# Performance work log

Measured on AMD Instinct MI355X. Metric: run time of the kernel, lower is better.

The kernel has to match this reference:

```python
import jax, jax.numpy as jnp
import numpy as np

N_STATE = 2048
N_HEAD = 16
HEAD_DIM = N_STATE // N_HEAD  # 128
ROPE_THETA = 10000.0


def setup_inputs() -> dict:
    key = jax.random.key(0)
    ks = jax.random.split(key, 8)
    B, S, D = 2, 2048, N_STATE
    scale = 1.0 / np.sqrt(D)
    x = jax.random.normal(ks[0], (B, S, D), dtype=jnp.float32)
    Wq = jax.random.normal(ks[1], (D, D), dtype=jnp.float32) * scale
    bq = jnp.zeros((D,), dtype=jnp.float32)
    Wk = jax.random.normal(ks[2], (D, D), dtype=jnp.float32) * scale  # key has no bias
    Wv = jax.random.normal(ks[3], (D, D), dtype=jnp.float32) * scale
    bv = jnp.zeros((D,), dtype=jnp.float32)
    Wo = jax.random.normal(ks[4], (D, D), dtype=jnp.float32) * scale
    bo = jnp.zeros((D,), dtype=jnp.float32)
    return {"x": x, "Wq": Wq, "bq": bq, "Wk": Wk, "Wv": Wv, "bv": bv, "Wo": Wo, "bo": bo}


def _rope(t, pos):
    # t: [B, S, H, hd]; torchtune-style interleaved rotary (pairs of adjacent dims)
    hd = t.shape[-1]
    inv_freq = 1.0 / (ROPE_THETA ** (jnp.arange(0, hd, 2, dtype=jnp.float32) / hd))  # [hd/2]
    ang = pos[:, None] * inv_freq[None, :]                    # [S, hd/2]
    cos = jnp.cos(ang)[None, :, None, :].astype(t.dtype)       # [1,S,1,hd/2]
    sin = jnp.sin(ang)[None, :, None, :].astype(t.dtype)
    t1 = t[..., 0::2]
    t2 = t[..., 1::2]
    rot = jnp.stack([t1 * cos - t2 * sin, t2 * cos + t1 * sin], axis=-1)
    return rot.reshape(t.shape)


def reference(x, Wq, bq, Wk, Wv, bv, Wo, bo):
    B, S, D = x.shape
    H, hd = N_HEAD, D // N_HEAD
    q = (x @ Wq.T + bq).reshape(B, S, H, hd)
    k = (x @ Wk.T).reshape(B, S, H, hd)
    v = (x @ Wv.T + bv).reshape(B, S, H, hd)
    pos = jnp.arange(S, dtype=jnp.float32)
    q = _rope(q, pos)
    k = _rope(k, pos)
    # [B,H,S,hd]
    q = q.transpose(0, 2, 1, 3)
    k = k.transpose(0, 2, 1, 3)
    v = v.transpose(0, 2, 1, 3)
    scale = 1.0 / jnp.sqrt(jnp.asarray(hd, dtype=x.dtype))
    scores = jnp.einsum('bhqd,bhkd->bhqk', q, k) * scale       # [B,H,S,S]
    causal = jnp.tril(jnp.ones((S, S), dtype=bool))
    scores = jnp.where(causal[None, None], scores, jnp.finfo(scores.dtype).min)
    probs = jax.nn.softmax(scores, axis=-1)
    a = jnp.einsum('bhqk,bhkd->bhqd', probs, v)                # [B,H,S,hd]
    a = a.transpose(0, 2, 1, 3).reshape(B, S, D)
    return a @ Wo.T + bo
```

## Files before the change

kernel.cpp:

```cpp
#include <hip/hip_runtime.h>
#include <stdint.h>

typedef float f32x4 __attribute__((ext_vector_type(4)));
typedef __bf16 bf16x8 __attribute__((ext_vector_type(8)));
typedef unsigned short us8 __attribute__((ext_vector_type(8)));
typedef unsigned short us4 __attribute__((ext_vector_type(4)));
typedef unsigned int u32;

#define MFMA16(A, B, C) __builtin_amdgcn_mfma_f32_16x16x32_bf16( \
    __builtin_bit_cast(bf16x8, (A)), __builtin_bit_cast(bf16x8, (B)), (C), 0, 0, 0)

__device__ __forceinline__ unsigned short f2bf(float f) {
  u32 u = __builtin_bit_cast(u32, f);
  u = u + 0x7fffu + ((u >> 16) & 1u);
  return (unsigned short)(u >> 16);
}
__device__ __forceinline__ float bf2f(unsigned short b) {
  u32 u = ((u32)b) << 16;
  return __builtin_bit_cast(float, u);
}
__device__ __forceinline__ void gload16(const void* g, void* lds) {
  __builtin_amdgcn_global_load_lds((const __attribute__((address_space(1))) u32*)g,
                                   (__attribute__((address_space(3))) u32*)lds, 16, 0, 0);
}

__global__ __launch_bounds__(256) void convert_all(
    const float* __restrict__ x, const float* __restrict__ wq, const float* __restrict__ wk,
    const float* __restrict__ wv, const float* __restrict__ wo,
    unsigned short* __restrict__ xb, unsigned short* __restrict__ wcat,
    unsigned short* __restrict__ wob) {
  int tid = blockIdx.x * 256 + threadIdx.x;
  int nth = gridDim.x * 256;
  const float* srcs[5] = {x, wq, wk, wv, wo};
  unsigned short* dsts[5] = {xb, wcat, wcat + 4194304, wcat + 8388608, wob};
  const int n4s[5] = {2097152, 1048576, 1048576, 1048576, 1048576};
#pragma unroll
  for (int sg = 0; sg < 5; ++sg) {
    const float4* s = (const float4*)srcs[sg];
    us4* d = (us4*)dsts[sg];
    int n4 = n4s[sg];
    for (int i = tid; i < n4; i += nth) {
      float4 v = s[i];
      us4 o;
      o[0] = f2bf(v.x); o[1] = f2bf(v.y); o[2] = f2bf(v.z); o[3] = f2bf(v.w);
      d[i] = o;
    }
  }
}

template <int EPI>
__global__ __launch_bounds__(512, 2) void gemm8(
    const unsigned short* __restrict__ A, const unsigned short* __restrict__ B,
    int nTN, int N,
    float* __restrict__ outF, const float* __restrict__ bias,
    unsigned short* __restrict__ qb, unsigned short* __restrict__ kb,
    unsigned short* __restrict__ vtb, const float* __restrict__ bq,
    const float* __restrict__ bv) {
  constexpr int KT = 32;
  __shared__ alignas(16) char L[131072];
  char* Lp = L;
  int bid = (int)blockIdx.x, nwg = (int)gridDim.x;
  {
    int qq = nwg >> 3;
    int xcd = bid & 7, idx = bid >> 3;
    bid = xcd * qq + idx;
  }
  int tm = bid / nTN, tn = bid % nTN;
  int t = (int)threadIdx.x, l = t & 63, w = t >> 6;
  int g = l >> 4, ln = l & 15;
  int wr = w >> 2, wc = w & 3;
  const unsigned short* pA = A + (size_t)(tm * 256 + l) * 2048 + w * 8;
  const unsigned short* pB = B + (size_t)(tn * 256 + l) * 2048 + w * 8;

  f32x4 acc[2][2][4][2] = {};
  us8 af[4][2], bf[2][2][2];

#define FENCE asm volatile("" ::: "memory")
#define BAR do { FENCE; __builtin_amdgcn_s_barrier(); FENCE; } while (0)
#define VMW_(n) asm volatile("s_waitcnt vmcnt(" #n ")" ::: "memory")
#define VMW(n) VMW_(n)
#define HT(op, h, kt, bufsel) do { if ((kt) < KT) {                           \
    char* lb = Lp + (bufsel) * 65536 + (op) * 32768 + (h) * 16384 + w * 2048; \
    const unsigned short* gs = ((op) ? pB : pA) +                             \
        (size_t)((h) * 128) * 2048 + (size_t)(kt) * 64;                       \
    gload16(gs, lb);                                                          \
    gload16(gs + (size_t)64 * 2048, lb + 1024);                               \
  } } while (0)
#define RD_A(mh_, bufsel) do {                                                \
    _Pragma("unroll") for (int mf = 0; mf < 4; ++mf)                          \
    _Pragma("unroll") for (int kc = 0; kc < 2; ++kc)                          \
      af[mf][kc] = *(const us8*)(Lp + (bufsel) * 65536 + wr * 16384 +         \
          (kc * 4 + g) * 2048 + ((mh_) * 64 + mf * 16 + ln) * 16);            \
  } while (0)
#define RD_B(nh_, bufsel) do {                                                \
    _Pragma("unroll") for (int nf = 0; nf < 2; ++nf)                          \
    _Pragma("unroll") for (int kc = 0; kc < 2; ++kc)                          \
      bf[nh_][nf][kc] = *(const us8*)(Lp + (bufsel) * 65536 + 32768 +         \
          (wc >> 1) * 16384 + (kc * 4 + g) * 2048 +                           \
          ((wc & 1) * 64 + (nh_) * 32 + nf * 16 + ln) * 16);                  \
  } while (0)
#define MM(mh_, nh_) do {                                                     \
    __builtin_amdgcn_s_setprio(1);                                            \
    _Pragma("unroll") for (int mf = 0; mf < 4; ++mf)                          \
    _Pragma("unroll") for (int nf = 0; nf < 2; ++nf)                          \
    _Pragma("unroll") for (int kc = 0; kc < 2; ++kc)                          \
      acc[mh_][nh_][mf][nf] = MFMA16(af[mf][kc], bf[nh_][nf][kc],             \
                                     acc[mh_][nh_][mf][nf]);                  \
    __builtin_amdgcn_s_setprio(0);                                            \
  } while (0)
#define TILE(kt, b, VM) do {                                                  \
   RD_A(0, b); RD_B(0, b); RD_B(1, b);                                 \
          HT(0, 1, (kt) + 1, (b) ^ 1);                                        \
          BAR; MM(0, 0); BAR;                                                 \
   HT(1, 0, (kt) + 2, b);                                              \
          BAR; MM(0, 1); BAR;                                                 \
   RD_A(1, b);                                                         \
          HT(1, 1, (kt) + 2, b);                                              \
          BAR; MM(1, 0); BAR;                                                 \
   HT(0, 0, (kt) + 2, b);                                              \
          MM(1, 1); VMW(VM); BAR;                                             \
} while (0)

  HT(0, 0, 0, 0); HT(1, 0, 0, 0); HT(1, 1, 0, 0);
  HT(0, 1, 0, 0); HT(1, 0, 1, 1); HT(1, 1, 1, 1); HT(0, 0, 1, 1);
  VMW(6); BAR;

#pragma unroll 1
  for (int it = 0; it < 15; ++it) {
    TILE(2 * it, 0, 6);
    TILE(2 * it + 1, 1, 6);
  }
  TILE(30, 0, 0);
  TILE(31, 1, 0);

#undef TILE
#undef MM
#undef RD_B
#undef RD_A
#undef HT
#undef VMW
#undef VMW_
#undef BAR
#undef FENCE

  if (EPI == 1) {
#pragma unroll
    for (int mh = 0; mh < 2; ++mh)
#pragma unroll
    for (int nh = 0; nh < 2; ++nh)
#pragma unroll
    for (int mf = 0; mf < 4; ++mf)
#pragma unroll
    for (int nf = 0; nf < 2; ++nf) {
      int n = tn * 256 + wc * 64 + nh * 32 + nf * 16 + ln;
      float bz = bias[n];
      int m0 = tm * 256 + wr * 128 + mh * 64 + mf * 16 + g * 4;
#pragma unroll
      for (int r = 0; r < 4; ++r)
        outF[(size_t)(m0 + r) * N + n] = acc[mh][nh][mf][nf][r] + bz;
    }
  } else {
#pragma unroll
    for (int mh = 0; mh < 2; ++mh)
#pragma unroll
    for (int nh = 0; nh < 2; ++nh)
#pragma unroll
    for (int mf = 0; mf < 4; ++mf)
#pragma unroll
    for (int nf = 0; nf < 2; ++nf) {
      int n6 = tn * 256 + wc * 64 + nh * 32 + nf * 16 + ln;
      int sel = n6 >> 11, d = n6 & 2047, h = d >> 7, hd = d & 127;
      int m0 = tm * 256 + wr * 128 + mh * 64 + mf * 16 + g * 4;
      int b = m0 >> 11, s0 = m0 & 2047;
      if (sel == 2) {
        float badd = bv[d];
        us4 pk;
#pragma unroll
        for (int r = 0; r < 4; ++r) pk[r] = f2bf(acc[mh][nh][mf][nf][r] + badd);
        *(us4*)&vtb[((size_t)(b * 16 + h) * 128 + hd) * 2048 + s0] = pk;
      } else {
        unsigned short* dst = sel ? kb : qb;
        float badd = sel ? 0.f : bq[d];
#pragma unroll
        for (int r = 0; r < 4; ++r)
          dst[((size_t)(b * 16 + h) * 2048 + (s0 + r)) * 128 + hd] =
              f2bf(acc[mh][nh][mf][nf][r] + badd);
      }
    }
  }
}

template <int EPI>
__global__ __launch_bounds__(512, 2) void gemm2(
    const unsigned short* __restrict__ A, const unsigned short* __restrict__ B,
    int nTN, int N,
    float* __restrict__ outF, const float* __restrict__ bias) {
  constexpr int K = 2048, KT = 64;
  __shared__ alignas(16) char L[4 * 24576];
  int bid = (int)blockIdx.x, nwg = (int)gridDim.x;
  {
    int qq = nwg >> 3;
    int xcd = bid & 7, idx = bid >> 3;
    bid = xcd * qq + idx;
  }
  int tm = bid / nTN, tn = bid % nTN;
  int t = (int)threadIdx.x, l = t & 63, w = t >> 6;
  int g = l >> 4, ln = l & 15;
  int wr = w >> 2, wc = w & 3;
  const unsigned short* Ab =
      A + (size_t)(tm * 128 + w * 16 + (l >> 2)) * K + (l & 3) * 8;
  const unsigned short* Bb =
      B + (size_t)(tn * 256 + w * 16 + (l >> 2)) * K + (l & 3) * 8;
  f32x4 acc[4][4] = {};

#define STAGE(tile) do {                                                      \
    char* Lb = L + ((tile) & 3) * 24576 + w * 1024;                           \
    int kc = (tile) * 32;                                                     \
    gload16(Ab + kc, Lb);                                                     \
    gload16(Bb + kc, Lb + 8192);                                              \
    gload16(Bb + (size_t)128 * K + kc, Lb + 16384);                           \
  } while (0)

#define GITER(kt, VM) do {                                                    \
    asm volatile("s_waitcnt vmcnt(" #VM ")" ::: "memory");                    \
    __builtin_amdgcn_s_barrier();                                             \
    __builtin_amdgcn_sched_barrier(0);                                        \
    asm volatile("" ::: "memory");                                            \
    if ((kt) + 3 < KT) STAGE((kt) + 3);                                       \
    const unsigned short* Lc = (const unsigned short*)(L + ((kt) & 3) * 24576); \
    us8 af[4], bfr[4];                                                        \
    _Pragma("unroll") for (int mf = 0; mf < 4; ++mf)                          \
      af[mf] = *(const us8*)&Lc[(wr * 64 + mf * 16 + ln) * 32 + g * 8];       \
    _Pragma("unroll") for (int nf = 0; nf < 4; ++nf)                          \
      bfr[nf] = *(const us8*)&Lc[4096 + (wc * 64 + nf * 16 + ln) * 32 + g * 8]; \
    __builtin_amdgcn_s_setprio(1);                                            \
    _Pragma("unroll") for (int mf = 0; mf < 4; ++mf)                          \
      _Pragma("unroll") for (int nf = 0; nf < 4; ++nf)                        \
        acc[mf][nf] = MFMA16(af[mf], bfr[nf], acc[mf][nf]);                   \
    __builtin_amdgcn_s_setprio(0);                                            \
  } while (0)

  STAGE(0); STAGE(1); STAGE(2);
#pragma unroll 1
  for (int kt = 0; kt < KT - 2; ++kt) GITER(kt, 6);
  GITER(KT - 2, 3);
  GITER(KT - 1, 0);
#undef STAGE
#undef GITER

#pragma unroll
  for (int mf = 0; mf < 4; ++mf)
#pragma unroll
    for (int nf = 0; nf < 4; ++nf) {
      int n = tn * 256 + wc * 64 + nf * 16 + ln;
      float bz = bias[n];
#pragma unroll
      for (int r = 0; r < 4; ++r) {
        int m = tm * 128 + wr * 64 + mf * 16 + g * 4 + r;
        outF[(size_t)m * N + n] = acc[mf][nf][r] + bz;
      }
    }
}

__global__ __launch_bounds__(256) void rope_k(u32* __restrict__ q, u32* __restrict__ k) {
  int idx = blockIdx.x * 256 + threadIdx.x;
  int i = idx & 63;
  int s = (idx >> 6) & 2047;
  float ang = (float)s * exp2f(-(float)i * 0.2076205059304703f);
  float sv, cv;
  sincosf(ang, &sv, &cv);
  u32 qu = q[idx];
  float a0 = bf2f((unsigned short)(qu & 0xffff)), a1 = bf2f((unsigned short)(qu >> 16));
  q[idx] = (u32)f2bf(a0 * cv - a1 * sv) | ((u32)f2bf(a1 * cv + a0 * sv) << 16);
  u32 ku = k[idx];
  float b0 = bf2f((unsigned short)(ku & 0xffff)), b1 = bf2f((unsigned short)(ku >> 16));
  k[idx] = (u32)f2bf(b0 * cv - b1 * sv) | ((u32)f2bf(b1 * cv + b0 * sv) << 16);
}

__global__ __launch_bounds__(512) void attn_k(
    const unsigned short* __restrict__ qg, const unsigned short* __restrict__ kg,
    const unsigned short* __restrict__ vtg, unsigned short* __restrict__ ab) {
  __shared__ alignas(16) unsigned short Kl[64 * 128];
  __shared__ alignas(16) unsigned short Vl[128 * 64];
  __shared__ alignas(16) unsigned short Pl[8][16 * 72];
  int bh = (int)blockIdx.x & 31;
  int pr = (int)blockIdx.x >> 5;
  int t = (int)threadIdx.x, l = t & 63, w = t >> 6;
  int g = l >> 4, ln = l & 15;
  int b = bh >> 4, h = bh & 15;
  const size_t bq0 = (size_t)bh * 2048 * 128;

#pragma unroll 1
  for (int half = 0; half < 2; ++half) {
    int qt = half ? 15 - pr : pr;
    int qbase = qt * 128;
    int qrow = qbase + w * 16 + ln;
    us8 qf[4];
#pragma unroll
    for (int kf = 0; kf < 4; ++kf)
      qf[kf] = *(const us8*)&qg[bq0 + (size_t)qrow * 128 + kf * 32 + g * 8];
    f32x4 o[8] = {};
    float mrow = -1e30f, lrow = 0.f;
    int nkt = (qbase >> 6) + 2;
#pragma unroll 1
    for (int kt = 0; kt < nkt; ++kt) {
      __syncthreads();
#pragma unroll
      for (int i = 0; i < 2; ++i) {
        int fb = i * 8192 + w * 1024;
        int flat = fb + l * 16;
        int row = flat >> 8, colb = flat & 255;
        int sc = colb ^ ((row & 7) << 4);
        gload16(kg + (bq0 + (size_t)(kt * 64 + row) * 128 + (sc >> 1)), (char*)Kl + fb);
        int rv = flat >> 7, cv2 = flat & 127;
        int scv = cv2 ^ ((rv & 7) << 4);
        gload16(vtg + (bq0 + (size_t)rv * 2048 + kt * 64 + (scv >> 1)), (char*)Vl + fb);
      }
      __syncthreads();
      f32x4 st[4];
#pragma unroll
      for (int kfr = 0; kfr < 4; ++kfr) {
        f32x4 acc = {};
        int row = kfr * 16 + ln;
        int swz = (row & 7) << 4;
#pragma unroll
        for (int kf = 0; kf < 4; ++kf) {
          us8 kfrag = *(const us8*)((const char*)Kl + row * 256 + ((kf * 64 + g * 16) ^ swz));
          acc = MFMA16(kfrag, qf[kf], acc);
        }
        st[kfr] = acc;
      }
      float pmax = -1e30f;
#pragma unroll
      for (int kfr = 0; kfr < 4; ++kfr)
#pragma unroll
        for (int r = 0; r < 4; ++r) {
          int key = kt * 64 + kfr * 16 + g * 4 + r;
          float sv = key <= qrow ? st[kfr][r] * 0.08838834764831845f : -1e30f;
          st[kfr][r] = sv;
          pmax = fmaxf(pmax, sv);
        }
      pmax = fmaxf(pmax, __shfl_xor(pmax, 16));
      pmax = fmaxf(pmax, __shfl_xor(pmax, 32));
      if (__ballot(pmax > mrow + 8.f)) {
        float mnew = pmax > mrow + 8.f ? pmax : mrow;
        float corr = exp2f((mrow - mnew) * 1.44269504f);
        mrow = mnew;
        lrow *= corr;
#pragma unroll
        for (int r = 0; r < 4; ++r) {
          float cr = __shfl(corr, g * 4 + r);
#pragma unroll
          for (int nf = 0; nf < 8; ++nf) o[nf][r] *= cr;
        }
      }
      float lsum = 0.f;
#pragma unroll
      for (int kfr = 0; kfr < 4; ++kfr) {
        us4 pk;
#pragma unroll
        for (int r = 0; r < 4; ++r) {
          float p = exp2f((st[kfr][r] - mrow) * 1.44269504f);
          lsum += p;
          pk[r] = f2bf(p);
        }
        *(us4*)&Pl[w][ln * 72 + kfr * 16 + g * 4] = pk;
      }
      lsum += __shfl_xor(lsum, 16);
      lsum += __shfl_xor(lsum, 32);
      lrow += lsum;
#pragma unroll
      for (int kf2 = 0; kf2 < 2; ++kf2) {
        us8 pa = *(const us8*)&Pl[w][ln * 72 + kf2 * 32 + g * 8];
#pragma unroll
        for (int nf = 0; nf < 8; ++nf) {
          int row = nf * 16 + ln;
          us8 vb = *(const us8*)((const char*)Vl + row * 128 +
                                 ((kf2 * 64 + g * 16) ^ ((row & 7) << 4)));
          o[nf] = MFMA16(pa, vb, o[nf]);
        }
      }
    }
    float invl = 1.f / lrow;
#pragma unroll
    for (int r = 0; r < 4; ++r) {
      float ir = __shfl(invl, g * 4 + r);
      int srow = qbase + w * 16 + g * 4 + r;
      size_t base = ((size_t)b * 2048 + srow) * 2048 + h * 128 + ln;
#pragma unroll
      for (int nf = 0; nf < 8; ++nf) ab[base + (size_t)nf * 16] = f2bf(o[nf][r] * ir);
    }
  }
}

extern "C" void kernel_launch(void* const* d_in, const int* in_sizes, int n_in,
                              void* d_out, int out_size, void* d_ws, size_t ws_size,
                              hipStream_t stream) {
  const float* x  = (const float*)d_in[0];
  const float* Wq = (const float*)d_in[1];
  const float* bq = (const float*)d_in[2];
  const float* Wk = (const float*)d_in[3];
  const float* Wv = (const float*)d_in[4];
  const float* bv = (const float*)d_in[5];
  const float* Wo = (const float*)d_in[6];
  const float* bo = (const float*)d_in[7];
  float* out = (float*)d_out;

  unsigned short* ws = (unsigned short*)d_ws;
  unsigned short* xb   = ws;
  unsigned short* wcat = xb + 8388608;
  unsigned short* wob  = wcat + 12582912;
  unsigned short* qb   = wob + 4194304;
  unsigned short* kb   = qb + 8388608;
  unsigned short* vtb  = kb + 8388608;

  convert_all<<<2048, 256, 0, stream>>>(x, Wq, Wk, Wv, Wo, xb, wcat, wob);
  gemm8<0><<<384, 512, 0, stream>>>(xb, wcat, 24, 6144,
                                    nullptr, nullptr, qb, kb, vtb, bq, bv);
  rope_k<<<16384, 256, 0, stream>>>((u32*)qb, (u32*)kb);
  attn_k<<<256, 512, 0, stream>>>(qb, kb, vtb, xb );
  gemm2<1><<<256, 512, 0, stream>>>(xb, wob, 8, 2048, out, bo);
}
```

Measured before the change: 299.8 us.

## Use XOR-swizzled row-major LDS layout and one-tile-ahead prefetch in QKV GEMM

The QKV projection GEMM now stages A and B tiles in LDS as row-major 128-byte rows, with a 16-byte chunk XOR swizzle applied on both the global-to-LDS load and the fragment reads. This replaces the old k-chunk-major layout and is meant to reduce LDS bank conflicts and improve global coalescing. The prefetch schedule also changes: the whole next tile is loaded into the other buffer during the current one, instead of staggering half-tiles two steps ahead. The waitcnt points move accordingly, and the shallower pipeline could expose more load latency.

```diff
diff --git a/kernel.cpp b/kernel.cpp
--- a/kernel.cpp
+++ b/kernel.cpp
@@ -49,7 +49,7 @@
 }
 
 template <int EPI>
-__global__ __launch_bounds__(512, 2) void gemm8(
+__global__ __launch_bounds__(512, 2) void gemmsw(
     const unsigned short* __restrict__ A, const unsigned short* __restrict__ B,
     int nTN, int N,
     float* __restrict__ outF, const float* __restrict__ bias,
@@ -69,8 +69,10 @@
   int t = (int)threadIdx.x, l = t & 63, w = t >> 6;
   int g = l >> 4, ln = l & 15;
   int wr = w >> 2, wc = w & 3;
-  const unsigned short* pA = A + (size_t)(tm * 256 + l) * 2048 + w * 8;
-  const unsigned short* pB = B + (size_t)(tn * 256 + l) * 2048 + w * 8;
+  int lr = l >> 3, lc = l & 7;
+  int scol = lc ^ lr;
+  const unsigned short* pAs = A + (size_t)(tm * 256 + w * 8 + lr) * 2048 + scol * 8;
+  const unsigned short* pBs = B + (size_t)(tn * 256 + w * 8 + lr) * 2048 + scol * 8;
 
   f32x4 acc[2][2][4][2] = {};
   us8 af[4][2], bf[2][2][2];
@@ -79,25 +81,25 @@
 #define BAR do { FENCE; __builtin_amdgcn_s_barrier(); FENCE; } while (0)
 #define VMW_(n) asm volatile("s_waitcnt vmcnt(" #n ")" ::: "memory")
 #define VMW(n) VMW_(n)
-#define HT(op, h, kt, bufsel) do { if ((kt) < KT) {                           \
-    char* lb = Lp + (bufsel) * 65536 + (op) * 32768 + (h) * 16384 + w * 2048; \
-    const unsigned short* gs = ((op) ? pB : pA) +                             \
-        (size_t)((h) * 128) * 2048 + (size_t)(kt) * 64;                       \
-    gload16(gs, lb);                                                          \
-    gload16(gs + (size_t)64 * 2048, lb + 1024);                               \
-  } } while (0)
+#define STA(i, kt, bufsel) do { if ((kt) < KT)                                \
+    gload16(pAs + (size_t)(i) * 131072 + (size_t)(kt) * 64,                   \
+            Lp + (bufsel) * 65536 + (i) * 8192 + w * 1024); } while (0)
+#define STB(i, kt, bufsel) do { if ((kt) < KT)                                \
+    gload16(pBs + (size_t)(i) * 131072 + (size_t)(kt) * 64,                   \
+            Lp + (bufsel) * 65536 + 32768 + (i) * 8192 + w * 1024); } while (0)
 #define RD_A(mh_, bufsel) do {                                                \
     _Pragma("unroll") for (int mf = 0; mf < 4; ++mf)                          \
     _Pragma("unroll") for (int kc = 0; kc < 2; ++kc)                          \
-      af[mf][kc] = *(const us8*)(Lp + (bufsel) * 65536 + wr * 16384 +         \
-          (kc * 4 + g) * 2048 + ((mh_) * 64 + mf * 16 + ln) * 16);            \
+      af[mf][kc] = *(const us8*)(Lp + (bufsel) * 65536 +                      \
+          (wr * 128 + (mh_) * 64 + mf * 16 + ln) * 128 +                      \
+          ((kc * 64 + g * 16) ^ ((ln & 7) << 4)));                            \
   } while (0)
 #define RD_B(nh_, bufsel) do {                                                \
     _Pragma("unroll") for (int nf = 0; nf < 2; ++nf)                          \
     _Pragma("unroll") for (int kc = 0; kc < 2; ++kc)                          \
       bf[nh_][nf][kc] = *(const us8*)(Lp + (bufsel) * 65536 + 32768 +         \
-          (wc >> 1) * 16384 + (kc * 4 + g) * 2048 +                           \
-          ((wc & 1) * 64 + (nh_) * 32 + nf * 16 + ln) * 16);                  \
+          (wc * 64 + (nh_) * 32 + nf * 16 + ln) * 128 +                       \
+          ((kc * 64 + g * 16) ^ ((ln & 7) << 4)));                            \
   } while (0)
 #define MM(mh_, nh_) do {                                                     \
     __builtin_amdgcn_s_setprio(1);                                            \
@@ -108,36 +110,37 @@
                                      acc[mh_][nh_][mf][nf]);                  \
     __builtin_amdgcn_s_setprio(0);                                            \
   } while (0)
-#define TILE(kt, b, VM) do {                                                  \
+#define TILE(kt, b, VM1, VM3) do {                                            \
    RD_A(0, b); RD_B(0, b); RD_B(1, b);                                 \
-          HT(0, 1, (kt) + 1, (b) ^ 1);                                        \
+          STB(0, (kt) + 1, (b) ^ 1); STB(1, (kt) + 1, (b) ^ 1);               \
           BAR; MM(0, 0); BAR;                                                 \
-   HT(1, 0, (kt) + 2, b);                                              \
-          BAR; MM(0, 1); BAR;                                                 \
+   STB(2, (kt) + 1, (b) ^ 1); STB(3, (kt) + 1, (b) ^ 1);               \
+          BAR; MM(0, 1); VMW(VM1); BAR;                                       \
    RD_A(1, b);                                                         \
-          HT(1, 1, (kt) + 2, b);                                              \
+          STA(0, (kt) + 1, (b) ^ 1); STA(2, (kt) + 1, (b) ^ 1);               \
           BAR; MM(1, 0); BAR;                                                 \
-   HT(0, 0, (kt) + 2, b);                                              \
-          MM(1, 1); VMW(VM); BAR;                                             \
+   STA(1, (kt) + 1, (b) ^ 1); STA(3, (kt) + 1, (b) ^ 1);               \
+          MM(1, 1); VMW(VM3); BAR;                                            \
 } while (0)
 
-  HT(0, 0, 0, 0); HT(1, 0, 0, 0); HT(1, 1, 0, 0);
-  HT(0, 1, 0, 0); HT(1, 0, 1, 1); HT(1, 1, 1, 1); HT(0, 0, 1, 1);
-  VMW(6); BAR;
+  STB(0, 0, 0); STB(1, 0, 0); STB(2, 0, 0); STB(3, 0, 0);
+  STA(0, 0, 0); STA(2, 0, 0); STA(1, 0, 0); STA(3, 0, 0);
+  VMW(0); BAR;
 
 #pragma unroll 1
-  for (int it = 0; it < 15; ++it) {
-    TILE(2 * it, 0, 6);
-    TILE(2 * it + 1, 1, 6);
-  }
-  TILE(30, 0, 0);
-  TILE(31, 1, 0);
+  for (int kt = 0; kt < 30; kt += 2) {
+    TILE(kt, 0, 4, 2);
+    TILE(kt + 1, 1, 4, 2);
+  }
+  TILE(30, 0, 4, 2);
+  TILE(31, 1, 0, 0);
 
 #undef TILE
 #undef MM
 #undef RD_B
 #undef RD_A
-#undef HT
+#undef STB
+#undef STA
 #undef VMW
 #undef VMW_
 #undef BAR
@@ -415,8 +418,8 @@
   unsigned short* vtb  = kb + 8388608;
 
   convert_all<<<2048, 256, 0, stream>>>(x, Wq, Wk, Wv, Wo, xb, wcat, wob);
-  gemm8<0><<<384, 512, 0, stream>>>(xb, wcat, 24, 6144,
-                                    nullptr, nullptr, qb, kb, vtb, bq, bv);
+  gemmsw<0><<<384, 512, 0, stream>>>(xb, wcat, 24, 6144,
+                                     nullptr, nullptr, qb, kb, vtb, bq, bv);
   rope_k<<<16384, 256, 0, stream>>>((u32*)qb, (u32*)kb);
   attn_k<<<256, 512, 0, stream>>>(qb, kb, vtb, xb );
   gemm2<1><<<256, 512, 0, stream>>>(xb, wob, 8, 2048, out, bo);
```

Result: faster. 275.6 us (-8.1%).
